# Performance work log

Measured on AMD Instinct MI355X. Metric: run time of the kernel, lower is better.

## Reference

```python
import jax, jax.numpy as jnp
import numpy as np

H = 187          # BATTLEFIELD_HEXES
MS = 20          # MAX_STACKS
MOB = 10         # MAX_OBSTACLES
D = 128          # d_model
NH = 4           # n_heads
NL = 4           # n_layers
CE = 16          # creature_embed_dim
NAT = 5          # NUM_ACTION_TYPES
NCT = 256        # NUM_CREATURE_TYPES
HEXC = 29        # HEX_CONTINUOUS_DIM
B = 1024


def _ln(x, g, b):
    m = x.mean(-1, keepdims=True)
    v = jnp.mean((x - m) ** 2, -1, keepdims=True)
    return (x - m) / jnp.sqrt(v + 1e-5) * g + b


def _mlp(x, w1, b1, w2, b2):
    return jax.nn.relu(x @ w1.T + b1) @ w2.T + b2


def _forward(p, n_stacks):
    scalars = p['scalars']
    s = p['stacks']
    pos = s[:, :, 18].astype(jnp.int32)                       # POSITION
    alive = s[:, :, 23]                                       # ALIVE
    idx_mask = jnp.arange(MS)[None, :] < n_stacks             # (B, MS)
    valid = (pos >= 0) & (pos < H) & (alive >= 0.5) & idx_mask
    max_hp = jnp.maximum(s[:, :, 4], 1.0)
    is_active = (s[:, :, 0] == scalars[:, 2:3]).astype(jnp.float32)
    is_ally = (s[:, :, 20] == scalars[:, 3:4]).astype(jnp.float32)
    zeros = jnp.zeros_like(alive)
    feat = jnp.stack([
        jnp.ones_like(alive), s[:, :, 2] / 1000.0, s[:, :, 3] / max_hp,
        s[:, :, 8] / 100.0, s[:, :, 9] / 100.0, s[:, :, 10] / 100.0, s[:, :, 11] / 100.0,
        s[:, :, 12] / 100.0, s[:, :, 13] / 100.0, s[:, :, 14] / 100.0, s[:, :, 15] / 100.0,
        s[:, :, 16] / 20.0, s[:, :, 17] / 20.0, s[:, :, 20], is_ally, alive,
        s[:, :, 24], s[:, :, 25], s[:, :, 26], s[:, :, 27], s[:, :, 28], s[:, :, 29],
        s[:, :, 30], s[:, :, 31] / 30.0, s[:, :, 33] / 5.0, s[:, :, 34] / 10.0,
        is_active, zeros, zeros], axis=-1)                    # (B, MS, 29)
    bidx = jnp.arange(B)[:, None]
    safe_pos = jnp.where(valid, pos, H)                       # dummy slot H for invalid
    hex_cont = jnp.zeros((B, H + 1, HEXC)).at[bidx, safe_pos].set(
        jnp.where(valid[..., None], feat, 0.0))[:, :H]
    cid = jnp.minimum(s[:, :, 1].astype(jnp.int32), NCT - 1)
    cids = jnp.zeros((B, H + 1), jnp.int32).at[bidx, safe_pos].set(
        jnp.where(valid, cid, 0))[:, :H]
    hex_cont = hex_cont.at[:, :, 27].set(p['reachable_hexes'])
    opos = p['obstacles'][:, :, 2].astype(jnp.int32)
    ovalid = (p['obstacles'][:, :, 0] > 0) & (opos >= 0) & (opos < H)
    obs_ch = jnp.zeros((B, H + 1)).at[bidx, jnp.where(ovalid, opos, H)].max(
        ovalid.astype(jnp.float32))[:, :H]
    hex_cont = hex_cont.at[:, :, 28].set(obs_ch)
    hex_feat = jnp.concatenate([hex_cont, p['creature_emb'][cids]], -1)   # (B,H,45)

    hex_tok = _ln(hex_feat @ p['hex_proj_w'].T + p['hex_proj_b'],
                  p['hex_ln_g'], p['hex_ln_b'])
    hex_tok = hex_tok + p['hex_pos_emb'][None] + p['tok_type_emb'][0]

    sc = scalars
    atk = jnp.stack([sc[:, 8], sc[:, 11] / 300.0, sc[:, 10] / 10.0, sc[:, 12] / 10.0,
                     jnp.zeros(B)], -1)
    dfn = jnp.stack([sc[:, 14], sc[:, 17] / 300.0, sc[:, 16] / 10.0, sc[:, 18] / 10.0,
                     jnp.ones(B)], -1)
    atk_t = _ln(atk @ p['hero_proj_w'].T + p['hero_proj_b'], p['hero_ln_g'], p['hero_ln_b']) + p['tok_type_emb'][1]
    def_t = _ln(dfn @ p['hero_proj_w'].T + p['hero_proj_b'], p['hero_ln_g'], p['hero_ln_b']) + p['tok_type_emb'][2]
    tokens = jnp.concatenate([hex_tok, atk_t[:, None], def_t[:, None]], 1)  # (B,189,D)

    gfeat = jnp.stack([sc[:, 1] / 50.0, sc[:, 4] / 10.0, sc[:, 5] / 10.0, sc[:, 6], sc[:, 3]], -1)
    tokens = tokens + (gfeat @ p['global_w'].T + p['global_b'])[:, None]

    S = tokens.shape[1]
    hd = D // NH
    for l in range(NL):  # pre-LN transformer encoder (eval mode, no dropout)
        x = _ln(tokens, p['tf_ln1_g'][l], p['tf_ln1_b'][l])
        qkv = x @ p['tf_qkv_w'][l].T + p['tf_qkv_b'][l]
        q, k, v = jnp.split(qkv, 3, -1)
        rs = lambda t: t.reshape(B, S, NH, hd).transpose(0, 2, 1, 3)
        q, k, v = rs(q), rs(k), rs(v)
        att = jax.nn.softmax(jnp.einsum('bhqd,bhkd->bhqk', q, k) / jnp.sqrt(float(hd)), -1)
        o = jnp.einsum('bhqk,bhkd->bhqd', att, v).transpose(0, 2, 1, 3).reshape(B, S, D)
        tokens = tokens + o @ p['tf_o_w'][l].T + p['tf_o_b'][l]
        y = _ln(tokens, p['tf_ln2_g'][l], p['tf_ln2_b'][l])
        tokens = tokens + jax.nn.relu(y @ p['tf_ff1_w'][l].T + p['tf_ff1_b'][l]) @ p['tf_ff2_w'][l].T + p['tf_ff2_b'][l]
    tokens = _ln(tokens, p['post_ln_g'], p['post_ln_b'])

    hex_out = tokens[:, :H]
    pooled = tokens.mean(1)
    action_type_logits = _mlp(pooled, p['at_w1'], p['at_b1'], p['at_w2'], p['at_b2'])
    hex_logits = _mlp(hex_out, p['hex_w1'], p['hex_b1'], p['hex_w2'], p['hex_b2']).squeeze(-1)
    tgt_tok = jnp.take_along_axis(hex_out, jnp.clip(pos, 0, H - 1)[..., None], axis=1)  # (B,MS,D)
    tgt = _mlp(tgt_tok, p['tg_w1'], p['tg_b1'], p['tg_w2'], p['tg_b2']).squeeze(-1)
    target_logits = jnp.where(valid, tgt, -1e9)
    value = _mlp(pooled, p['val_w1'], p['val_b1'], p['val_w2'], p['val_b2']).squeeze(-1)
    return (action_type_logits, hex_logits, target_logits, value)


def setup_inputs() -> dict:
    key = jax.random.key(0)
    ks = iter(jax.random.split(key, 64))
    nk = lambda: next(ks)
    _p = lambda shape: 0.02 * jax.random.normal(nk(), shape, dtype=jnp.float32)

    scalars = jax.random.uniform(nk(), (B, 19)) * 10.0
    scalars = scalars.at[:, 2].set(jax.random.randint(nk(), (B,), 0, MS).astype(jnp.float32))
    scalars = scalars.at[:, 3].set(jax.random.randint(nk(), (B,), 0, 2).astype(jnp.float32))

    stacks = jax.random.uniform(nk(), (B, MS, 35)) * 50.0
    perm = jax.vmap(lambda k: jax.random.permutation(k, H)[:MS])(jax.random.split(nk(), B))
    stacks = stacks.at[:, :, 18].set(perm.astype(jnp.float32))          # unique positions
    stacks = stacks.at[:, :, 23].set((jax.random.uniform(nk(), (B, MS)) > 0.2).astype(jnp.float32))
    stacks = stacks.at[:, :, 1].set(jax.random.randint(nk(), (B, MS), 0, NCT).astype(jnp.float32))
    stacks = stacks.at[:, :, 0].set(jnp.broadcast_to(jnp.arange(MS, dtype=jnp.float32), (B, MS)))
    stacks = stacks.at[:, :, 20].set(jax.random.randint(nk(), (B, MS), 0, 2).astype(jnp.float32))

    obstacles = jnp.stack([
        jax.random.randint(nk(), (B, MOB), 0, 3).astype(jnp.float32),
        jnp.zeros((B, MOB)),
        jax.random.randint(nk(), (B, MOB), 0, H).astype(jnp.float32)], -1)
    reachable_hexes = (jax.random.uniform(nk(), (B, H)) > 0.5).astype(jnp.float32)
    n_stacks = jax.random.randint(nk(), (B, 1), 1, MS + 1)

    inp = dict(scalars=scalars, stacks=stacks, obstacles=obstacles,
               reachable_hexes=reachable_hexes, n_stacks=n_stacks)
    inp['creature_emb'] = _p((NCT, CE)).at[0].set(0.0)   # padding_idx=0
    inp['hex_pos_emb'] = _p((H, D))
    inp['tok_type_emb'] = _p((3, D))
    inp['hex_proj_w'] = _p((D, HEXC + CE)); inp['hex_proj_b'] = _p((D,))
    inp['hex_ln_g'] = jnp.ones(D); inp['hex_ln_b'] = jnp.zeros(D)
    inp['hero_proj_w'] = _p((D, 5)); inp['hero_proj_b'] = _p((D,))
    inp['hero_ln_g'] = jnp.ones(D); inp['hero_ln_b'] = jnp.zeros(D)
    inp['global_w'] = _p((D, 5)); inp['global_b'] = _p((D,))
    inp['tf_ln1_g'] = jnp.ones((NL, D)); inp['tf_ln1_b'] = jnp.zeros((NL, D))
    inp['tf_qkv_w'] = _p((NL, 3 * D, D)); inp['tf_qkv_b'] = _p((NL, 3 * D))
    inp['tf_o_w'] = _p((NL, D, D)); inp['tf_o_b'] = _p((NL, D))
    inp['tf_ln2_g'] = jnp.ones((NL, D)); inp['tf_ln2_b'] = jnp.zeros((NL, D))
    inp['tf_ff1_w'] = _p((NL, 4 * D, D)); inp['tf_ff1_b'] = _p((NL, 4 * D))
    inp['tf_ff2_w'] = _p((NL, D, 4 * D)); inp['tf_ff2_b'] = _p((NL, D))
    inp['post_ln_g'] = jnp.ones(D); inp['post_ln_b'] = jnp.zeros(D)
    inp['at_w1'] = _p((D, D)); inp['at_b1'] = _p((D,)); inp['at_w2'] = _p((NAT, D)); inp['at_b2'] = _p((NAT,))
    inp['hex_w1'] = _p((D // 2, D)); inp['hex_b1'] = _p((D // 2,)); inp['hex_w2'] = _p((1, D // 2)); inp['hex_b2'] = _p((1,))
    inp['tg_w1'] = _p((D // 2, D)); inp['tg_b1'] = _p((D // 2,)); inp['tg_w2'] = _p((1, D // 2)); inp['tg_b2'] = _p((1,))
    inp['val_w1'] = _p((D, D)); inp['val_b1'] = _p((D,)); inp['val_w2'] = _p((1, D)); inp['val_b2'] = _p((1,))
    return inp


def reference(scalars, stacks, obstacles, reachable_hexes, n_stacks, creature_emb, hex_pos_emb, tok_type_emb, hex_proj_w, hex_proj_b, hex_ln_g, hex_ln_b, hero_proj_w, hero_proj_b, hero_ln_g, hero_ln_b, global_w, global_b, tf_ln1_g, tf_ln1_b, tf_qkv_w, tf_qkv_b, tf_o_w, tf_o_b, tf_ln2_g, tf_ln2_b, tf_ff1_w, tf_ff1_b, tf_ff2_w, tf_ff2_b, post_ln_g, post_ln_b, at_w1, at_b1, at_w2, at_b2, hex_w1, hex_b1, hex_w2, hex_b2, tg_w1, tg_b1, tg_w2, tg_b2, val_w1, val_b1, val_w2, val_b2):
    fl = dict(locals())
    ns = fl.pop('n_stacks')
    return _forward(fl, ns)
```

## Files before the change

kernel.cpp:

```cpp
#include <hip/hip_runtime.h>
#include <hip/hip_bf16.h>

#define DEV static __device__ __forceinline__

typedef __attribute__((ext_vector_type(8))) short bf16x8;
typedef __attribute__((ext_vector_type(4))) float f32x4;
#define MFMA16 __builtin_amdgcn_mfma_f32_16x16x32_bf16

DEV unsigned short f2bf_rn(float x) {
  unsigned u = __float_as_uint(x);
  u = u + 0x7fffu + ((u >> 16) & 1u);
  return (unsigned short)(u >> 16);
}
DEV unsigned pack2(float a, float b) {
  return (unsigned)f2bf_rn(a) | ((unsigned)f2bf_rn(b) << 16);
}
DEV float lo2f(unsigned w) { return __uint_as_float(w << 16); }
DEV float hi2f(unsigned w) { return __uint_as_float(w & 0xffff0000u); }

constexpr int H_ = 187, MS_ = 20, MOB_ = 10, D_ = 128, NH_ = 4, NL_ = 4,
              CE_ = 16, NAT_ = 5, NCT_ = 256, HEXC_ = 29, B_ = 1024;
constexpr int S_ = H_ + 2;
constexpr int ST = 68;
constexpr int PST = 36;
// ... 16 lines not shown
constexpr int WS_Q = 0;
constexpr int WS_O = WS_Q + 4 * 384 * 128;
constexpr int WS_F1 = WS_O + 4 * 128 * 128;
constexpr int WS_F2 = WS_F1 + 4 * 512 * 128;
constexpr int WS_TOT = WS_F2 + 4 * 128 * 512;

struct Params {
  const float *scalars, *stacks, *obstacles, *reach;
  const int  *n_stacks;
  const float *cemb, *pos_emb, *tte;
  const float *hexW, *hexB, *hexG, *hexBe;
  const float *heroW, *heroB, *heroG, *heroBe;
  const float *gW, *gB;
  const float *ln1g, *ln1b, *qkvW, *qkvB, *oW, *oB;
  const float *ln2g, *ln2b, *f1W, *f1B, *f2W, *f2B;
  const float *plng, *plnb;
  const float *atW1, *atB1, *atW2, *atB2;
  const float *hxW1, *hxB1, *hxW2, *hxB2;
  const float *tgW1, *tgB1, *tgW2, *tgB2;
  const float *vlW1, *vlB1, *vlW2, *vlB2;
  const unsigned short *wsb;
  float *out;
};

DEV bf16x8 ldAx(const unsigned* buf, int stride, int mbase, int cbase, int lane) {
  return *(const bf16x8*)(buf + (mbase + (lane & 15)) * stride + cbase +
                          ((lane >> 4) << 2));
}
DEV bf16x8 ldBw(const float* q) {
  bf16x8 r;
#pragma unroll
  for (int j = 0; j < 8; ++j) r[j] = (short)f2bf_rn(q[j]);
  return r;
}
template <bool WSB>
DEV bf16x8 ldB(const unsigned short* wb, const float* wf, int off) {
  if constexpr (WSB) return *(const bf16x8*)(wb + off);
  else return ldBw(wf + off);
}

__global__ __launch_bounds__(256) void convw_kernel(const float *qkv,
                                                    const float *o,
                                                    const float *f1,
                                                    const float *f2,
                                                    unsigned short *ws) {
  int i = blockIdx.x * 256 + threadIdx.x;
  if (i < WS_O) ws[i] = f2bf_rn(qkv[i - WS_Q]);
  else if (i < WS_F1) ws[i] = f2bf_rn(o[i - WS_O]);
  else if (i < WS_F2) ws[i] = f2bf_rn(f1[i - WS_F1]);
  else if (i < WS_TOT) ws[i] = f2bf_rn(f2[i - WS_F2]);
}

template <bool WSB>
__global__ __launch_bounds__(384, 1) void battle_kernel(Params p) {
  __shared__ __align__(16) unsigned tokp[192 * ST];
  __shared__ __align__(16) unsigned xln[192 * ST];
  __shared__ __align__(16) unsigned area[192 * ST];
  __shared__ int svalid[MS_], sposc[MS_];

  const int b = blockIdx.x;
  const int tid = threadIdx.x;
  const int lane = tid & 63;
  const int wave = tid >> 6;
  const bool hasrow = tid < S_;
  const float *sc = p.scalars + b * 19;

  float *areaF = (float *)area;
  unsigned short *tok16 = (unsigned short *)tokp;
  unsigned short *xln16 = (unsigned short *)xln;
  unsigned short *P16 = (unsigned short *)area;
  unsigned short *vt16 = (unsigned short *)(area + VT_OFF);

  float *hexcont = (float *)area;
  int   *cids    = (int *)area + 5440;
  float *obsch   = (float *)area + 5632;

  if (tid < D_) {
    float g0 = sc[1] * 0.02f, g1 = sc[4] * 0.1f, g2 = sc[5] * 0.1f;
    float g3 = sc[6], g4 = sc[3];
    const float *w = p.gW + tid * 5;
    areaF[GV_OFF + tid] = p.gB[tid] + g0 * w[0] + g1 * w[1] + g2 * w[2] +
                          g3 * w[3] + g4 * w[4];
  }
  for (int i = tid; i < H_ * HEXC_; i += 384) hexcont[i] = 0.f;
  for (int i = tid; i < H_; i += 384) { cids[i] = 0; obsch[i] = 0.f; }
  if (tid >= 189 && tid < 192) {
    for (int c = 0; c < 64; ++c) tokp[tid * ST + c] = 0u;
  }
  __syncthreads();

  if (tid < MS_) {
    const float *st = p.stacks + (b * MS_ + tid) * 35;
    int pos = (int)st[18];
    float alive = st[23];
    int ns = p.n_stacks[b];
    bool valid = (pos >= 0) && (pos < H_) && (alive >= 0.5f) && (tid < ns);
    svalid[tid] = valid ? 1 : 0;
    sposc[tid] = min(max(pos, 0), H_ - 1);
    if (valid) {
      float maxhp = fmaxf(st[4], 1.0f);
      float *hc = hexcont + pos * HEXC_;
      hc[0] = 1.0f;
      hc[1] = st[2] * 1e-3f;
      hc[2] = st[3] / maxhp;
      hc[3] = st[8] * 0.01f;  hc[4] = st[9] * 0.01f;
      hc[5] = st[10] * 0.01f; hc[6] = st[11] * 0.01f;
      hc[7] = st[12] * 0.01f; hc[8] = st[13] * 0.01f;
      hc[9] = st[14] * 0.01f; hc[10] = st[15] * 0.01f;
      hc[11] = st[16] * 0.05f; hc[12] = st[17] * 0.05f;
      float s20 = st[20];
      hc[13] = s20;
      hc[14] = (s20 == sc[3]) ? 1.f : 0.f;
      hc[15] = alive;
      hc[16] = st[24]; hc[17] = st[25]; hc[18] = st[26];
      hc[19] = st[27]; hc[20] = st[28]; hc[21] = st[29];
      hc[22] = st[30];
      hc[23] = st[31] * (1.f / 30.f);
      hc[24] = st[33] * 0.2f;
      hc[25] = st[34] * 0.1f;
      hc[26] = (st[0] == sc[2]) ? 1.f : 0.f;
      hc[27] = 0.f; hc[28] = 0.f;
      cids[pos] = min((int)st[1], NCT_ - 1);
    }
  }
  if (tid >= 64 && tid < 64 + MOB_) {
    const float *ob = p.obstacles + (b * MOB_ + (tid - 64)) * 3;
    int opos = (int)ob[2];
    if (ob[0] > 0.f && opos >= 0 && opos < H_) obsch[opos] = 1.0f;
  }
  __syncthreads();

  if (tid < H_) {
    const int r = tid;
    float f[HEXC_ + CE_];
#pragma unroll
    for (int c = 0; c < HEXC_; ++c) f[c] = hexcont[r * HEXC_ + c];
    f[27] = p.reach[b * H_ + r];
    f[28] = obsch[r];
// ... 27 lines not shown
      float t0 = lo2f(w) - m, t1 = hi2f(w) - m;
      var = fmaf(t0, t0, var); var = fmaf(t1, t1, var);
    }
    float rs = rsqrtf(var * (1.f / 128.f) + 1e-5f);
#pragma unroll 2
    for (int d2 = 0; d2 < 64; ++d2) {
      unsigned w = tokp[r * ST + d2];
      int d = 2 * d2;
      float v0 = (lo2f(w) - m) * rs * p.hexG[d] + p.hexBe[d] +
                 p.pos_emb[r * D_ + d] + p.tte[d] + areaF[GV_OFF + d];
      float v1 = (hi2f(w) - m) * rs * p.hexG[d + 1] + p.hexBe[d + 1] +
                 p.pos_emb[r * D_ + d + 1] + p.tte[d + 1] + areaF[GV_OFF + d + 1];
      tokp[r * ST + d2] = pack2(v0, v1);
    }
  } else if (tid < S_) {
    const int which = tid - H_;
    float f0, f1, f2, f3, f4;
    if (which == 0) {
      f0 = sc[8];  f1 = sc[11] * (1.f / 300.f);
      f2 = sc[10] * 0.1f; f3 = sc[12] * 0.1f; f4 = 0.f;
    } else {
      f0 = sc[14]; f1 = sc[17] * (1.f / 300.f);
      f2 = sc[16] * 0.1f; f3 = sc[18] * 0.1f; f4 = 1.f;
    }
    const int r = tid;
    float sum = 0.f;
    for (int d2 = 0; d2 < 64; ++d2) {
      const float *w0 = p.heroW + (2 * d2) * 5;
      const float *w1 = w0 + 5;
      float va = p.heroB[2 * d2] + f0 * w0[0] + f1 * w0[1] + f2 * w0[2] + f3 * w0[3] + f4 * w0[4];
      float vb = p.heroB[2 * d2 + 1] + f0 * w1[0] + f1 * w1[1] + f2 * w1[2] + f3 * w1[3] + f4 * w1[4];
      tokp[r * ST + d2] = pack2(va, vb);
      sum += va + vb;
    }
    float m = sum * (1.f / 128.f);
    float var = 0.f;
    for (int d2 = 0; d2 < 64; ++d2) {
      unsigned w = tokp[r * ST + d2];
      float t0 = lo2f(w) - m, t1 = hi2f(w) - m;
      var = fmaf(t0, t0, var); var = fmaf(t1, t1, var);
    }
    float rs = rsqrtf(var * (1.f / 128.f) + 1e-5f);
    for (int d2 = 0; d2 < 64; ++d2) {
      unsigned w = tokp[r * ST + d2];
      int d = 2 * d2;
      float v0 = (lo2f(w) - m) * rs * p.heroG[d] + p.heroBe[d] +
                 p.tte[(1 + which) * D_ + d] + areaF[GV_OFF + d];
      float v1 = (hi2f(w) - m) * rs * p.heroG[d + 1] + p.heroBe[d + 1] +
                 p.tte[(1 + which) * D_ + d + 1] + areaF[GV_OFF + d + 1];
      tokp[r * ST + d2] = pack2(v0, v1);
    }
  }

  for (int l = 0; l < NL_; ++l) {
    const float *ln1g = p.ln1g + l * D_, *ln1b = p.ln1b + l * D_;
    const float *qkvW = p.qkvW + l * 3 * D_ * D_, *qkvB = p.qkvB + l * 3 * D_;
    const float *oW = p.oW + l * D_ * D_, *oB = p.oB + l * D_;
    const float *ln2g = p.ln2g + l * D_, *ln2b = p.ln2b + l * D_;
    const float *f1W = p.f1W + l * 4 * D_ * D_, *f1B = p.f1B + l * 4 * D_;
    const float *f2W = p.f2W + l * 4 * D_ * D_, *f2B = p.f2B + l * D_;
    const unsigned short *qkvWb = p.wsb + WS_Q + l * 384 * 128;
    const unsigned short *oWb = p.wsb + WS_O + l * 128 * 128;
    const unsigned short *f1Wb = p.wsb + WS_F1 + l * 512 * 128;
    const unsigned short *f2Wb = p.wsb + WS_F2 + l * 128 * 512;

    __syncthreads();

    if (hasrow) {
      float s0 = 0.f, s1 = 0.f;
#pragma unroll 8
      for (int d2 = 0; d2 < 64; ++d2) {
        unsigned w = tokp[tid * ST + d2];
        s0 += lo2f(w); s1 += hi2f(w);
      }
      float m = (s0 + s1) * (1.f / 128.f);
      float v0 = 0.f, v1 = 0.f;
#pragma unroll 8
      for (int d2 = 0; d2 < 64; ++d2) {
        unsigned w = tokp[tid * ST + d2];
        float t0 = lo2f(w) - m, t1 = hi2f(w) - m;
        v0 = fmaf(t0, t0, v0); v1 = fmaf(t1, t1, v1);
      }
      float rs = rsqrtf((v0 + v1) * (1.f / 128.f) + 1e-5f);
#pragma unroll 2
      for (int d2 = 0; d2 < 64; ++d2) {
        unsigned w = tokp[tid * ST + d2];
        int d = 2 * d2;
        xln[tid * ST + d2] = pack2((lo2f(w) - m) * rs * ln1g[d] + ln1b[d],
                                   (hi2f(w) - m) * rs * ln1g[d + 1] + ln1b[d + 1]);
      }
    } else if (tid < 192) {
      for (int d2 = 0; d2 < 64; ++d2) xln[tid * ST + d2] = 0u;
    }
    __syncthreads();

    f32x4 oacc[4][2][2];

#pragma unroll
    for (int h = 0; h < NH_; ++h) {
#pragma unroll
      for (int mi = 0; mi < 2; ++mi)
#pragma unroll
        for (int nd = 0; nd < 2; ++nd) oacc[h][mi][nd] = {0.f, 0.f, 0.f, 0.f};

      {
        int job = wave;
        int nrow0, c16 = 0, isV = 0, ntd = 0;
        if (job < 2)      { nrow0 = h * 32 + job * 16;            c16 = job * 16; }
        else if (job < 4) { nrow0 = 128 + h * 32 + (job - 2) * 16; c16 = 32 + (job - 2) * 16; }
        else              { nrow0 = 256 + h * 32 + (job - 4) * 16; isV = 1; ntd = job - 4; }
        int roff = (nrow0 + (lane & 15)) * 128;
        int koff = (lane >> 4) << 3;
        bf16x8 b0 = ldB<WSB>(qkvWb, qkvW, roff + koff);
        bf16x8 b1 = ldB<WSB>(qkvWb, qkvW, roff + 32 + koff);
        bf16x8 b2 = ldB<WSB>(qkvWb, qkvW, roff + 64 + koff);
        bf16x8 b3 = ldB<WSB>(qkvWb, qkvW, roff + 96 + koff);
        float bv = qkvB[nrow0 + (lane & 15)];
        int col16 = c16 + (lane & 15);
#pragma unroll 1
        for (int mt = 0; mt < 12; ++mt) {
          f32x4 acc = {bv, bv, bv, bv};
          acc = MFMA16(ldAx(xln, ST, mt * 16, 0, lane), b0, acc, 0, 0, 0);
          acc = MFMA16(ldAx(xln, ST, mt * 16, 16, lane), b1, acc, 0, 0, 0);
          acc = MFMA16(ldAx(xln, ST, mt * 16, 32, lane), b2, acc, 0, 0, 0);
          acc = MFMA16(ldAx(xln, ST, mt * 16, 48, lane), b3, acc, 0, 0, 0);
          int rb = mt * 16 + ((lane >> 4) << 2);
          if (!isV) {
#pragma unroll
            for (int g = 0; g < 4; ++g)
              P16[(rb + g) * (PST * 2) + col16] = f2bf_rn(acc[g]);
          } else {
#pragma unroll
            for (int g = 0; g < 4; ++g)
              vt16[(ntd * 16 + (lane & 15)) * (VTS * 2) + rb + g] = f2bf_rn(acc[g]);
          }
        }
      }
      __syncthreads();

      bf16x8 qf0 = ldAx(area, PST, (2 * wave) * 16, 0, lane);
      bf16x8 qf1 = ldAx(area, PST, (2 * wave + 1) * 16, 0, lane);
      bf16x8 kf[12];
#pragma unroll
      for (int nt = 0; nt < 12; ++nt)
        kf[nt] = ldAx(area, PST, nt * 16, 16, lane);
      float mrun = -1e30f, lrun = 0.f;
      const int srow = 32 * wave + (lane & 31);
      const int shalf = lane >> 5;
      __syncthreads();

#pragma unroll
      for (int t = 0; t < 3; ++t) {
#pragma unroll
        for (int mi = 0; mi < 2; ++mi) {
          int rb = (2 * wave + mi) * 16 + ((lane >> 4) << 2);
#pragma unroll
          for (int ntl = 0; ntl < 4; ++ntl) {
            f32x4 s = {0.f, 0.f, 0.f, 0.f};
            s = MFMA16(mi ? qf1 : qf0, kf[t * 4 + ntl], s, 0, 0, 0);
            int col16 = ntl * 16 + (lane & 15);
#pragma unroll
            for (int g = 0; g < 4; ++g)
              P16[(rb + g) * (PST * 2) + col16] = f2bf_rn(s[g]);
          }
        }
        {
          float tm = -1e30f;
          int cb = shalf * 16;
#pragma unroll
          for (int c2i = 0; c2i < 16; ++c2i) {
            int c2 = cb + c2i;
            unsigned w = area[srow * PST + c2];
            float v0 = lo2f(w) * SCALE, v1 = hi2f(w) * SCALE;
            if (t == 2 && c2 == 30) v1 = -1e30f;
            if (t == 2 && c2 == 31) { v0 = -1e30f; v1 = -1e30f; }
            tm = fmaxf(tm, fmaxf(v0, v1));
          }
          tm = fmaxf(tm, __shfl_xor(tm, 32));
          float mnew = fmaxf(mrun, tm);
          float corrv = __expf(mrun - mnew);
          float ts = 0.f;
#pragma unroll
          for (int c2i = 0; c2i < 16; ++c2i) {
            int c2 = cb + c2i;
            unsigned w = area[srow * PST + c2];
            float e0 = __expf(lo2f(w) * SCALE - mnew);
            float e1 = __expf(hi2f(w) * SCALE - mnew);
            if (t == 2 && c2 == 30) e1 = 0.f;
            if (t == 2 && c2 == 31) { e0 = 0.f; e1 = 0.f; }
            ts += e0 + e1;
            area[srow * PST + c2] = pack2(e0, e1);
          }
          ts += __shfl_xor(ts, 32);
          lrun = lrun * corrv + ts;
          mrun = mnew;
          if (shalf == 0) {
            areaF[CORR_OFF + srow] = corrv;
            if (t == 2) areaF[LSUM_OFF + srow] = lrun;
          }
        }
#pragma unroll
        for (int mi = 0; mi < 2; ++mi) {
          int rb = (2 * wave + mi) * 16 + ((lane >> 4) << 2);
          float c0 = areaF[CORR_OFF + rb], c1 = areaF[CORR_OFF + rb + 1];
          float c2v = areaF[CORR_OFF + rb + 2], c3 = areaF[CORR_OFF + rb + 3];
#pragma unroll
          for (int nd = 0; nd < 2; ++nd) {
            f32x4 a = oacc[h][mi][nd];
            a[0] *= c0; a[1] *= c1; a[2] *= c2v; a[3] *= c3;
#pragma unroll
            for (int kt = 0; kt < 2; ++kt) {
              bf16x8 af = ldAx(area, PST, (2 * wave + mi) * 16, kt * 16, lane);
              bf16x8 bv = *(const bf16x8*)(area + VT_OFF +
                            (nd * 16 + (lane & 15)) * VTS + t * 32 + kt * 16 +
                            ((lane >> 4) << 2));
              a = MFMA16(af, bv, a, 0, 0, 0);
            }
            oacc[h][mi][nd] = a;
          }
          if (t == 2) {
            float i0 = 1.f / areaF[LSUM_OFF + rb];
            float i1 = 1.f / areaF[LSUM_OFF + rb + 1];
            float i2 = 1.f / areaF[LSUM_OFF + rb + 2];
            float i3 = 1.f / areaF[LSUM_OFF + rb + 3];
#pragma unroll
            for (int nd = 0; nd < 2; ++nd) {
              f32x4 a = oacc[h][mi][nd];
              a[0] *= i0; a[1] *= i1; a[2] *= i2; a[3] *= i3;
              oacc[h][mi][nd] = a;
            }
          }
        }
      }
      __syncthreads();
    }

#pragma unroll
    for (int h = 0; h < NH_; ++h)
#pragma unroll
      for (int mi = 0; mi < 2; ++mi) {
        int rb = (2 * wave + mi) * 16 + ((lane >> 4) << 2);
#pragma unroll
        for (int nd = 0; nd < 2; ++nd) {
          int col16 = h * 32 + nd * 16 + (lane & 15);
          f32x4 a = oacc[h][mi][nd];
#pragma unroll
          for (int g = 0; g < 4; ++g)
            xln16[(rb + g) * (ST * 2) + col16] = f2bf_rn(a[g]);
        }
      }
    __syncthreads();

#pragma unroll 1
    for (int job = wave; job < 16; job += 6) {
      int nt = job >> 1, mh = job & 1;
      int roff = (nt * 16 + (lane & 15)) * 128;
      int koff = (lane >> 4) << 3;
      bf16x8 b0 = ldB<WSB>(oWb, oW, roff + koff);
      bf16x8 b1 = ldB<WSB>(oWb, oW, roff + 32 + koff);
      bf16x8 b2 = ldB<WSB>(oWb, oW, roff + 64 + koff);
      bf16x8 b3 = ldB<WSB>(oWb, oW, roff + 96 + koff);
      float bv = oB[nt * 16 + (lane & 15)];
      int col16 = nt * 16 + (lane & 15);
#pragma unroll 1
      for (int mt = mh * 6; mt < mh * 6 + 6; ++mt) {
        f32x4 acc = {bv, bv, bv, bv};
        acc = MFMA16(ldAx(xln, ST, mt * 16, 0, lane), b0, acc, 0, 0, 0);
        acc = MFMA16(ldAx(xln, ST, mt * 16, 16, lane), b1, acc, 0, 0, 0);
        acc = MFMA16(ldAx(xln, ST, mt * 16, 32, lane), b2, acc, 0, 0, 0);
        acc = MFMA16(ldAx(xln, ST, mt * 16, 48, lane), b3, acc, 0, 0, 0);
        int rb = mt * 16 + ((lane >> 4) << 2);
#pragma unroll
        for (int g = 0; g < 4; ++g) {
          int a16 = (rb + g) * (ST * 2) + col16;
          float old = __uint_as_float((unsigned)tok16[a16] << 16);
          tok16[a16] = f2bf_rn(old + acc[g]);
        }
      }
    }
    __syncthreads();

    if (hasrow) {
      float s0 = 0.f, s1 = 0.f;
#pragma unroll 8
      for (int d2 = 0; d2 < 64; ++d2) {
        unsigned w = tokp[tid * ST + d2];
        s0 += lo2f(w); s1 += hi2f(w);
      }
      float m = (s0 + s1) * (1.f / 128.f);
      float v0 = 0.f, v1 = 0.f;
#pragma unroll 8
      for (int d2 = 0; d2 < 64; ++d2) {
        unsigned w = tokp[tid * ST + d2];
        float t0 = lo2f(w) - m, t1 = hi2f(w) - m;
        v0 = fmaf(t0, t0, v0); v1 = fmaf(t1, t1, v1);
      }
      float rs = rsqrtf((v0 + v1) * (1.f / 128.f) + 1e-5f);
#pragma unroll 2
      for (int d2 = 0; d2 < 64; ++d2) {
        unsigned w = tokp[tid * ST + d2];
        int d = 2 * d2;
        xln[tid * ST + d2] = pack2((lo2f(w) - m) * rs * ln2g[d] + ln2b[d],
                                   (hi2f(w) - m) * rs * ln2g[d + 1] + ln2b[d + 1]);
      }
    } else if (tid < 192) {
      for (int d2 = 0; d2 < 64; ++d2) xln[tid * ST + d2] = 0u;
    }
    __syncthreads();

    f32x4 acc2[2][12];
#pragma unroll
    for (int o = 0; o < 2; ++o) {
      int nt = wave + 6 * o;
      float bv = (nt < 8) ? f2B[nt * 16 + (lane & 15)] : 0.f;
#pragma unroll
      for (int mt = 0; mt < 12; ++mt) acc2[o][mt] = {bv, bv, bv, bv};
    }
    for (int chunk = 0; chunk < 4; ++chunk) {
#pragma unroll 1
      for (int job = wave; job < 16; job += 6) {
        int nt = job >> 1, mh = job & 1;
        int roff = (chunk * 128 + nt * 16 + (lane & 15)) * 128;
        int koff = (lane >> 4) << 3;
        bf16x8 b0 = ldB<WSB>(f1Wb, f1W, roff + koff);
        bf16x8 b1 = ldB<WSB>(f1Wb, f1W, roff + 32 + koff);
        bf16x8 b2 = ldB<WSB>(f1Wb, f1W, roff + 64 + koff);
        bf16x8 b3 = ldB<WSB>(f1Wb, f1W, roff + 96 + koff);
        float bv = f1B[chunk * 128 + nt * 16 + (lane & 15)];
        int col16 = nt * 16 + (lane & 15);
#pragma unroll 1
        for (int mt = mh * 6; mt < mh * 6 + 6; ++mt) {
          f32x4 acc = {bv, bv, bv, bv};
          acc = MFMA16(ldAx(xln, ST, mt * 16, 0, lane), b0, acc, 0, 0, 0);
          acc = MFMA16(ldAx(xln, ST, mt * 16, 16, lane), b1, acc, 0, 0, 0);
          acc = MFMA16(ldAx(xln, ST, mt * 16, 32, lane), b2, acc, 0, 0, 0);
          acc = MFMA16(ldAx(xln, ST, mt * 16, 48, lane), b3, acc, 0, 0, 0);
          int rb = mt * 16 + ((lane >> 4) << 2);
#pragma unroll
          for (int g = 0; g < 4; ++g)
            P16[(rb + g) * (ST * 2) + col16] = f2bf_rn(fmaxf(acc[g], 0.f));
        }
      }
      __syncthreads();
#pragma unroll
      for (int o = 0; o < 2; ++o) {
        int nt = wave + 6 * o;
        if (nt < 8) {
          int roff = (nt * 16 + (lane & 15)) * 512 + chunk * 128;
          int koff = (lane >> 4) << 3;
          bf16x8 b0 = ldB<WSB>(f2Wb, f2W, roff + koff);
          bf16x8 b1 = ldB<WSB>(f2Wb, f2W, roff + 32 + koff);
          bf16x8 b2 = ldB<WSB>(f2Wb, f2W, roff + 64 + koff);
          bf16x8 b3 = ldB<WSB>(f2Wb, f2W, roff + 96 + koff);
#pragma unroll
          for (int mt = 0; mt < 12; ++mt) {
            f32x4 a = acc2[o][mt];
            a = MFMA16(ldAx(area, ST, mt * 16, 0, lane), b0, a, 0, 0, 0);
            a = MFMA16(ldAx(area, ST, mt * 16, 16, lane), b1, a, 0, 0, 0);
            a = MFMA16(ldAx(area, ST, mt * 16, 32, lane), b2, a, 0, 0, 0);
            a = MFMA16(ldAx(area, ST, mt * 16, 48, lane), b3, a, 0, 0, 0);
            acc2[o][mt] = a;
          }
        }
      }
      __syncthreads();
    }
#pragma unroll
    for (int o = 0; o < 2; ++o) {
      int nt = wave + 6 * o;
      if (nt < 8) {
        int col16 = nt * 16 + (lane & 15);
#pragma unroll
        for (int mt = 0; mt < 12; ++mt) {
          int rb = mt * 16 + ((lane >> 4) << 2);
          f32x4 a = acc2[o][mt];
#pragma unroll
          for (int g = 0; g < 4; ++g) {
            int a16 = (rb + g) * (ST * 2) + col16;
            float old = __uint_as_float((unsigned)tok16[a16] << 16);
            tok16[a16] = f2bf_rn(old + a[g]);
          }
        }
      }
    }
  }
  __syncthreads();

  if (hasrow) {
    float s0 = 0.f, s1 = 0.f;
#pragma unroll 8
    for (int d2 = 0; d2 < 64; ++d2) {
      unsigned w = tokp[tid * ST + d2];
      s0 += lo2f(w); s1 += hi2f(w);
    }
    float m = (s0 + s1) * (1.f / 128.f);
    float v0 = 0.f, v1 = 0.f;
#pragma unroll 8
    for (int d2 = 0; d2 < 64; ++d2) {
      unsigned w = tokp[tid * ST + d2];
      float t0 = lo2f(w) - m, t1 = hi2f(w) - m;
      v0 = fmaf(t0, t0, v0); v1 = fmaf(t1, t1, v1);
    }
    float rs = rsqrtf((v0 + v1) * (1.f / 128.f) + 1e-5f);
#pragma unroll 2
    for (int d2 = 0; d2 < 64; ++d2) {
      unsigned w = tokp[tid * ST + d2];
      int d = 2 * d2;
      tokp[tid * ST + d2] = pack2((lo2f(w) - m) * rs * p.plng[d] + p.plnb[d],
                                  (hi2f(w) - m) * rs * p.plng[d + 1] + p.plnb[d + 1]);
    }
  }
  __syncthreads();

  if (tid < D_) {
    const int d2 = tid >> 1;
    const bool hi = tid & 1;
    float s0 = 0.f, s1 = 0.f;
    int r = 0;
    for (; r + 2 <= S_; r += 2) {
      unsigned w0 = tokp[r * ST + d2], w1 = tokp[(r + 1) * ST + d2];
      s0 += hi ? hi2f(w0) : lo2f(w0);
      s1 += hi ? hi2f(w1) : lo2f(w1);
    }
    unsigned wl = tokp[(S_ - 1) * ST + d2];
    s0 += hi ? hi2f(wl) : lo2f(wl);
    areaF[PO_OFF + tid] = (s0 + s1) * (1.f / (float)S_);
  }
  __syncthreads();
  if (tid < D_) {
    const float *wa = p.atW1 + tid * D_;
    const float *wv = p.vlW1 + tid * D_;
    float a0 = p.atB1[tid], a1 = 0.f, vv0 = p.vlB1[tid], vv1 = 0.f;
#pragma unroll 4
    for (int k = 0; k < D_; k += 2) {
      float pk0 = areaF[PO_OFF + k], pk1 = areaF[PO_OFF + k + 1];
      a0 = fmaf(pk0, wa[k], a0);   a1 = fmaf(pk1, wa[k + 1], a1);
      vv0 = fmaf(pk0, wv[k], vv0); vv1 = fmaf(pk1, wv[k + 1], vv1);
    }
    areaF[H1_OFF + tid] = fmaxf(a0 + a1, 0.f);
    areaF[H2_OFF + tid] = fmaxf(vv0 + vv1, 0.f);
  }
  __syncthreads();

  if (tid < H_) {
    float hh[64];
#pragma unroll
    for (int j = 0; j < 64; ++j) hh[j] = p.hxB1[j];
    for (int kb = 0; kb < 8; ++kb) {
      float xr[16];
#pragma unroll
      for (int i2 = 0; i2 < 8; ++i2) {
        unsigned w = tokp[tid * ST + kb * 8 + i2];
        xr[2 * i2] = lo2f(w); xr[2 * i2 + 1] = hi2f(w);
      }
      const float *w = p.hxW1 + kb * 16;
#pragma unroll
      for (int j = 0; j < 64; ++j) {
#pragma unroll
        for (int i = 0; i < 16; ++i)
          hh[j] = fmaf(xr[i], w[j * D_ + i], hh[j]);
      }
    }
// ... 47 lines not shown
          for (int i = 0; i < 16; ++i)
            hh[j] = fmaf(xr[i], w[j * D_ + i], hh[j]);
        }
      }
      o = p.tgB2[0];
#pragma unroll
      for (int j = 0; j < 64; ++j) o = fmaf(fmaxf(hh[j], 0.f), p.tgW2[j], o);
    } else {
      o = -1e9f;
    }
    p.out[OFF_TGT + b * MS_ + si] = o;
  }
}

extern "C" void kernel_launch(void* const* d_in, const int* in_sizes, int n_in,
                              void* d_out, int out_size, void* d_ws, size_t ws_size,
                              hipStream_t stream) {
  (void)in_sizes; (void)n_in; (void)out_size;
  Params p;
  p.scalars = (const float *)d_in[0];
  p.stacks = (const float *)d_in[1];
  p.obstacles = (const float *)d_in[2];
  p.reach = (const float *)d_in[3];
  p.n_stacks = (const int *)d_in[4];
  p.cemb = (const float *)d_in[5];
  p.pos_emb = (const float *)d_in[6];
  p.tte = (const float *)d_in[7];
  p.hexW = (const float *)d_in[8];  p.hexB = (const float *)d_in[9];
  p.hexG = (const float *)d_in[10]; p.hexBe = (const float *)d_in[11];
  p.heroW = (const float *)d_in[12]; p.heroB = (const float *)d_in[13];
  p.heroG = (const float *)d_in[14]; p.heroBe = (const float *)d_in[15];
  p.gW = (const float *)d_in[16]; p.gB = (const float *)d_in[17];
  p.ln1g = (const float *)d_in[18]; p.ln1b = (const float *)d_in[19];
  p.qkvW = (const float *)d_in[20]; p.qkvB = (const float *)d_in[21];
  p.oW = (const float *)d_in[22]; p.oB = (const float *)d_in[23];
  p.ln2g = (const float *)d_in[24]; p.ln2b = (const float *)d_in[25];
  p.f1W = (const float *)d_in[26]; p.f1B = (const float *)d_in[27];
  p.f2W = (const float *)d_in[28]; p.f2B = (const float *)d_in[29];
  p.plng = (const float *)d_in[30]; p.plnb = (const float *)d_in[31];
  p.atW1 = (const float *)d_in[32]; p.atB1 = (const float *)d_in[33];
  p.atW2 = (const float *)d_in[34]; p.atB2 = (const float *)d_in[35];
  p.hxW1 = (const float *)d_in[36]; p.hxB1 = (const float *)d_in[37];
  p.hxW2 = (const float *)d_in[38]; p.hxB2 = (const float *)d_in[39];
  p.tgW1 = (const float *)d_in[40]; p.tgB1 = (const float *)d_in[41];
  p.tgW2 = (const float *)d_in[42]; p.tgB2 = (const float *)d_in[43];
  p.vlW1 = (const float *)d_in[44]; p.vlB1 = (const float *)d_in[45];
  p.vlW2 = (const float *)d_in[46]; p.vlB2 = (const float *)d_in[47];
  p.out = (float *)d_out;
  bool usews = ws_size >= (size_t)WS_TOT * 2;
  if (usews) {
    p.wsb = (const unsigned short *)d_ws;
    convw_kernel<<<dim3((WS_TOT + 255) / 256), dim3(256), 0, stream>>>(
        p.qkvW, p.oW, p.f1W, p.f2W, (unsigned short *)d_ws);
    battle_kernel<true><<<dim3(B_), dim3(384), 0, stream>>>(p);
  } else {
    p.wsb = nullptr;
    battle_kernel<false><<<dim3(B_), dim3(384), 0, stream>>>(p);
  }
}
```

Before: 2.115 ms.

## Double block to 768 threads and repartition LN, attention and FFN work across 12 waves

Raises the block size from 384 to 768 threads, so 12 waves share each batch element instead of 6. LayerNorm now uses 4 threads per row with shuffle reductions rather than one thread per row. Attention gives each wave one 16-row tile, the QKV projection splits M tiles in half across wave pairs, and FF2 tiles are redistributed over 12 waves. This targets the serial per-row LayerNorm and low wave-level parallelism inside the block, at the cost of fewer registers per thread and more threads per barrier.

```diff
diff --git a/kernel.cpp b/kernel.cpp
--- a/kernel.cpp
+++ b/kernel.cpp
@@ -92,7 +92,7 @@
 }
 
 template <bool WSB>
-__global__ __launch_bounds__(384, 1) void battle_kernel(Params p) {
+__global__ __launch_bounds__(768, 1) void battle_kernel(Params p) {
   __shared__ __align__(16) unsigned tokp[192 * ST];
   __shared__ __align__(16) unsigned xln[192 * ST];
   __shared__ __align__(16) unsigned area[192 * ST];
@@ -122,8 +122,8 @@
     areaF[GV_OFF + tid] = p.gB[tid] + g0 * w[0] + g1 * w[1] + g2 * w[2] +
                           g3 * w[3] + g4 * w[4];
   }
-  for (int i = tid; i < H_ * HEXC_; i += 384) hexcont[i] = 0.f;
-  for (int i = tid; i < H_; i += 384) { cids[i] = 0; obsch[i] = 0.f; }
+  for (int i = tid; i < H_ * HEXC_; i += 768) hexcont[i] = 0.f;
+  for (int i = tid; i < H_; i += 768) { cids[i] = 0; obsch[i] = 0.f; }
   if (tid >= 189 && tid < 192) {
     for (int c = 0; c < 64; ++c) tokp[tid * ST + c] = 0u;
   }
@@ -257,6 +257,9 @@
     }
   }
 
+  const int lrow = tid >> 2;
+  const int lsub = tid & 3;
+
   for (int l = 0; l < NL_; ++l) {
     const float *ln1g = p.ln1g + l * D_, *ln1b = p.ln1b + l * D_;
     const float *qkvW = p.qkvW + l * 3 * D_ * D_, *qkvB = p.qkvB + l * 3 * D_;
@@ -271,49 +274,50 @@
 
     __syncthreads();
 
-    if (hasrow) {
-      float s0 = 0.f, s1 = 0.f;
-#pragma unroll 8
-      for (int d2 = 0; d2 < 64; ++d2) {
-        unsigned w = tokp[tid * ST + d2];
-        s0 += lo2f(w); s1 += hi2f(w);
-      }
-      float m = (s0 + s1) * (1.f / 128.f);
-      float v0 = 0.f, v1 = 0.f;
-#pragma unroll 8
-      for (int d2 = 0; d2 < 64; ++d2) {
-        unsigned w = tokp[tid * ST + d2];
+    if (lrow < S_) {
+      float s = 0.f;
+#pragma unroll
+      for (int i = 0; i < 16; ++i) {
+        unsigned w = tokp[lrow * ST + lsub * 16 + i];
+        s += lo2f(w) + hi2f(w);
+      }
+      s += __shfl_xor(s, 1); s += __shfl_xor(s, 2);
+      float m = s * (1.f / 128.f);
+      float v = 0.f;
+#pragma unroll
+      for (int i = 0; i < 16; ++i) {
+        unsigned w = tokp[lrow * ST + lsub * 16 + i];
         float t0 = lo2f(w) - m, t1 = hi2f(w) - m;
-        v0 = fmaf(t0, t0, v0); v1 = fmaf(t1, t1, v1);
-      }
-      float rs = rsqrtf((v0 + v1) * (1.f / 128.f) + 1e-5f);
-#pragma unroll 2
-      for (int d2 = 0; d2 < 64; ++d2) {
-        unsigned w = tokp[tid * ST + d2];
-        int d = 2 * d2;
-        xln[tid * ST + d2] = pack2((lo2f(w) - m) * rs * ln1g[d] + ln1b[d],
-                                   (hi2f(w) - m) * rs * ln1g[d + 1] + ln1b[d + 1]);
-      }
-    } else if (tid < 192) {
-      for (int d2 = 0; d2 < 64; ++d2) xln[tid * ST + d2] = 0u;
+        v = fmaf(t0, t0, v); v = fmaf(t1, t1, v);
+      }
+      v += __shfl_xor(v, 1); v += __shfl_xor(v, 2);
+      float rs = rsqrtf(v * (1.f / 128.f) + 1e-5f);
+#pragma unroll
+      for (int i = 0; i < 16; ++i) {
+        int d2 = lsub * 16 + i, d = 2 * d2;
+        unsigned w = tokp[lrow * ST + d2];
+        xln[lrow * ST + d2] = pack2((lo2f(w) - m) * rs * ln1g[d] + ln1b[d],
+                                    (hi2f(w) - m) * rs * ln1g[d + 1] + ln1b[d + 1]);
+      }
+    } else {
+#pragma unroll
+      for (int i = 0; i < 16; ++i) xln[lrow * ST + lsub * 16 + i] = 0u;
     }
     __syncthreads();
 
-    f32x4 oacc[4][2][2];
+    f32x4 oacc[4][2];
 
 #pragma unroll
     for (int h = 0; h < NH_; ++h) {
 #pragma unroll
-      for (int mi = 0; mi < 2; ++mi)
-#pragma unroll
-        for (int nd = 0; nd < 2; ++nd) oacc[h][mi][nd] = {0.f, 0.f, 0.f, 0.f};
+      for (int nd = 0; nd < 2; ++nd) oacc[h][nd] = {0.f, 0.f, 0.f, 0.f};
 
       {
-        int job = wave;
+        int ntg = wave >> 1, mh = wave & 1;
         int nrow0, c16 = 0, isV = 0, ntd = 0;
-        if (job < 2)      { nrow0 = h * 32 + job * 16;            c16 = job * 16; }
-        else if (job < 4) { nrow0 = 128 + h * 32 + (job - 2) * 16; c16 = 32 + (job - 2) * 16; }
-        else              { nrow0 = 256 + h * 32 + (job - 4) * 16; isV = 1; ntd = job - 4; }
+        if (ntg < 2)      { nrow0 = h * 32 + ntg * 16;            c16 = ntg * 16; }
+        else if (ntg < 4) { nrow0 = 128 + h * 32 + (ntg - 2) * 16; c16 = 32 + (ntg - 2) * 16; }
+        else              { nrow0 = 256 + h * 32 + (ntg - 4) * 16; isV = 1; ntd = ntg - 4; }
         int roff = (nrow0 + (lane & 15)) * 128;
         int koff = (lane >> 4) << 3;
         bf16x8 b0 = ldB<WSB>(qkvWb, qkvW, roff + koff);
@@ -323,7 +327,7 @@
         float bv = qkvB[nrow0 + (lane & 15)];
         int col16 = c16 + (lane & 15);
 #pragma unroll 1
-        for (int mt = 0; mt < 12; ++mt) {
+        for (int mt = mh * 6; mt < mh * 6 + 6; ++mt) {
           f32x4 acc = {bv, bv, bv, bv};
           acc = MFMA16(ldAx(xln, ST, mt * 16, 0, lane), b0, acc, 0, 0, 0);
           acc = MFMA16(ldAx(xln, ST, mt * 16, 16, lane), b1, acc, 0, 0, 0);
@@ -343,26 +347,24 @@
       }
       __syncthreads();
 
-      bf16x8 qf0 = ldAx(area, PST, (2 * wave) * 16, 0, lane);
-      bf16x8 qf1 = ldAx(area, PST, (2 * wave + 1) * 16, 0, lane);
+      bf16x8 qf = ldAx(area, PST, wave * 16, 0, lane);
       bf16x8 kf[12];
 #pragma unroll
       for (int nt = 0; nt < 12; ++nt)
         kf[nt] = ldAx(area, PST, nt * 16, 16, lane);
       float mrun = -1e30f, lrun = 0.f;
-      const int srow = 32 * wave + (lane & 31);
-      const int shalf = lane >> 5;
+      const int srow = wave * 16 + (lane & 15);
+      const int ssub = lane >> 4;
       __syncthreads();
 
 #pragma unroll
       for (int t = 0; t < 3; ++t) {
-#pragma unroll
-        for (int mi = 0; mi < 2; ++mi) {
-          int rb = (2 * wave + mi) * 16 + ((lane >> 4) << 2);
+        {
+          int rb = wave * 16 + ((lane >> 4) << 2);
 #pragma unroll
           for (int ntl = 0; ntl < 4; ++ntl) {
             f32x4 s = {0.f, 0.f, 0.f, 0.f};
-            s = MFMA16(mi ? qf1 : qf0, kf[t * 4 + ntl], s, 0, 0, 0);
+            s = MFMA16(qf, kf[t * 4 + ntl], s, 0, 0, 0);
             int col16 = ntl * 16 + (lane & 15);
 #pragma unroll
             for (int g = 0; g < 4; ++g)
@@ -371,23 +373,24 @@
         }
         {
           float tm = -1e30f;
-          int cb = shalf * 16;
-#pragma unroll
-          for (int c2i = 0; c2i < 16; ++c2i) {
-            int c2 = cb + c2i;
+          int cb = ssub * 8;
+#pragma unroll
+          for (int i = 0; i < 8; ++i) {
+            int c2 = cb + i;
             unsigned w = area[srow * PST + c2];
             float v0 = lo2f(w) * SCALE, v1 = hi2f(w) * SCALE;
             if (t == 2 && c2 == 30) v1 = -1e30f;
             if (t == 2 && c2 == 31) { v0 = -1e30f; v1 = -1e30f; }
             tm = fmaxf(tm, fmaxf(v0, v1));
           }
+          tm = fmaxf(tm, __shfl_xor(tm, 16));
           tm = fmaxf(tm, __shfl_xor(tm, 32));
           float mnew = fmaxf(mrun, tm);
           float corrv = __expf(mrun - mnew);
           float ts = 0.f;
 #pragma unroll
-          for (int c2i = 0; c2i < 16; ++c2i) {
-            int c2 = cb + c2i;
+          for (int i = 0; i < 8; ++i) {
+            int c2 = cb + i;
             unsigned w = area[srow * PST + c2];
             float e0 = __expf(lo2f(w) * SCALE - mnew);
             float e1 = __expf(hi2f(w) * SCALE - mnew);
@@ -396,32 +399,32 @@
             ts += e0 + e1;
             area[srow * PST + c2] = pack2(e0, e1);
           }
+          ts += __shfl_xor(ts, 16);
           ts += __shfl_xor(ts, 32);
           lrun = lrun * corrv + ts;
           mrun = mnew;
-          if (shalf == 0) {
+          if (ssub == 0) {
             areaF[CORR_OFF + srow] = corrv;
             if (t == 2) areaF[LSUM_OFF + srow] = lrun;
           }
         }
-#pragma unroll
-        for (int mi = 0; mi < 2; ++mi) {
-          int rb = (2 * wave + mi) * 16 + ((lane >> 4) << 2);
+        {
+          int rb = wave * 16 + ((lane >> 4) << 2);
           float c0 = areaF[CORR_OFF + rb], c1 = areaF[CORR_OFF + rb + 1];
           float c2v = areaF[CORR_OFF + rb + 2], c3 = areaF[CORR_OFF + rb + 3];
 #pragma unroll
           for (int nd = 0; nd < 2; ++nd) {
-            f32x4 a = oacc[h][mi][nd];
+            f32x4 a = oacc[h][nd];
             a[0] *= c0; a[1] *= c1; a[2] *= c2v; a[3] *= c3;
 #pragma unroll
             for (int kt = 0; kt < 2; ++kt) {
-              bf16x8 af = ldAx(area, PST, (2 * wave + mi) * 16, kt * 16, lane);
+              bf16x8 af = ldAx(area, PST, wave * 16, kt * 16, lane);
               bf16x8 bv = *(const bf16x8*)(area + VT_OFF +
                             (nd * 16 + (lane & 15)) * VTS + t * 32 + kt * 16 +
                             ((lane >> 4) << 2));
               a = MFMA16(af, bv, a, 0, 0, 0);
             }
-            oacc[h][mi][nd] = a;
+            oacc[h][nd] = a;
           }
           if (t == 2) {
             float i0 = 1.f / areaF[LSUM_OFF + rb];
@@ -430,9 +433,9 @@
             float i3 = 1.f / areaF[LSUM_OFF + rb + 3];
 #pragma unroll
             for (int nd = 0; nd < 2; ++nd) {
-              f32x4 a = oacc[h][mi][nd];
+              f32x4 a = oacc[h][nd];
               a[0] *= i0; a[1] *= i1; a[2] *= i2; a[3] *= i3;
-              oacc[h][mi][nd] = a;
+              oacc[h][nd] = a;
             }
           }
         }
@@ -441,23 +444,21 @@
     }
 
 #pragma unroll
-    for (int h = 0; h < NH_; ++h)
-#pragma unroll
-      for (int mi = 0; mi < 2; ++mi) {
-        int rb = (2 * wave + mi) * 16 + ((lane >> 4) << 2);
-#pragma unroll
-        for (int nd = 0; nd < 2; ++nd) {
-          int col16 = h * 32 + nd * 16 + (lane & 15);
-          f32x4 a = oacc[h][mi][nd];
-#pragma unroll
-          for (int g = 0; g < 4; ++g)
-            xln16[(rb + g) * (ST * 2) + col16] = f2bf_rn(a[g]);
-        }
-      }
+    for (int h = 0; h < NH_; ++h) {
+      int rb = wave * 16 + ((lane >> 4) << 2);
+#pragma unroll
+      for (int nd = 0; nd < 2; ++nd) {
+        int col16 = h * 32 + nd * 16 + (lane & 15);
+        f32x4 a = oacc[h][nd];
+#pragma unroll
+        for (int g = 0; g < 4; ++g)
+          xln16[(rb + g) * (ST * 2) + col16] = f2bf_rn(a[g]);
+      }
+    }
     __syncthreads();
 
 #pragma unroll 1
-    for (int job = wave; job < 16; job += 6) {
+    for (int job = wave; job < 16; job += 12) {
       int nt = job >> 1, mh = job & 1;
       int roff = (nt * 16 + (lane & 15)) * 128;
       int koff = (lane >> 4) << 3;
@@ -485,45 +486,54 @@
     }
     __syncthreads();
 
-    if (hasrow) {
-      float s0 = 0.f, s1 = 0.f;
-#pragma unroll 8
-      for (int d2 = 0; d2 < 64; ++d2) {
-        unsigned w = tokp[tid * ST + d2];
-        s0 += lo2f(w); s1 += hi2f(w);
-      }
-      float m = (s0 + s1) * (1.f / 128.f);
-      float v0 = 0.f, v1 = 0.f;
-#pragma unroll 8
-      for (int d2 = 0; d2 < 64; ++d2) {
-        unsigned w = tokp[tid * ST + d2];
+    if (lrow < S_) {
+      float s = 0.f;
+#pragma unroll
+      for (int i = 0; i < 16; ++i) {
+        unsigned w = tokp[lrow * ST + lsub * 16 + i];
+        s += lo2f(w) + hi2f(w);
+      }
+      s += __shfl_xor(s, 1); s += __shfl_xor(s, 2);
+      float m = s * (1.f / 128.f);
+      float v = 0.f;
+#pragma unroll
+      for (int i = 0; i < 16; ++i) {
+        unsigned w = tokp[lrow * ST + lsub * 16 + i];
         float t0 = lo2f(w) - m, t1 = hi2f(w) - m;
-        v0 = fmaf(t0, t0, v0); v1 = fmaf(t1, t1, v1);
-      }
-      float rs = rsqrtf((v0 + v1) * (1.f / 128.f) + 1e-5f);
-#pragma unroll 2
-      for (int d2 = 0; d2 < 64; ++d2) {
-        unsigned w = tokp[tid * ST + d2];
-        int d = 2 * d2;
-        xln[tid * ST + d2] = pack2((lo2f(w) - m) * rs * ln2g[d] + ln2b[d],
-                                   (hi2f(w) - m) * rs * ln2g[d + 1] + ln2b[d + 1]);
-      }
-    } else if (tid < 192) {
-      for (int d2 = 0; d2 < 64; ++d2) xln[tid * ST + d2] = 0u;
+        v = fmaf(t0, t0, v); v = fmaf(t1, t1, v);
+      }
+      v += __shfl_xor(v, 1); v += __shfl_xor(v, 2);
+      float rs = rsqrtf(v * (1.f / 128.f) + 1e-5f);
+#pragma unroll
+      for (int i = 0; i < 16; ++i) {
+        int d2 = lsub * 16 + i, d = 2 * d2;
+        unsigned w = tokp[lrow * ST + d2];
+        xln[lrow * ST + d2] = pack2((lo2f(w) - m) * rs * ln2g[d] + ln2b[d],
+                                    (hi2f(w) - m) * rs * ln2g[d + 1] + ln2b[d + 1]);
+      }
+    } else {
+#pragma unroll
+      for (int i = 0; i < 16; ++i) xln[lrow * ST + lsub * 16 + i] = 0u;
     }
     __syncthreads();
 
-    f32x4 acc2[2][12];
-#pragma unroll
-    for (int o = 0; o < 2; ++o) {
-      int nt = wave + 6 * o;
-      float bv = (nt < 8) ? f2B[nt * 16 + (lane & 15)] : 0.f;
-#pragma unroll
-      for (int mt = 0; mt < 12; ++mt) acc2[o][mt] = {bv, bv, bv, bv};
+    const int ja = wave;
+    const bool hasb = wave < 4;
+    const int jb = wave + 12;
+    const int nta = ja >> 1, mha = ja & 1;
+    const int ntb = jb >> 1, mhb = jb & 1;
+    f32x4 acca[6], accb[6];
+    {
+      float bva = f2B[nta * 16 + (lane & 15)];
+#pragma unroll
+      for (int i = 0; i < 6; ++i) acca[i] = {bva, bva, bva, bva};
+      float bvb = hasb ? f2B[ntb * 16 + (lane & 15)] : 0.f;
+#pragma unroll
+      for (int i = 0; i < 6; ++i) accb[i] = {bvb, bvb, bvb, bvb};
     }
     for (int chunk = 0; chunk < 4; ++chunk) {
 #pragma unroll 1
-      for (int job = wave; job < 16; job += 6) {
+      for (int job = wave; job < 16; job += 12) {
         int nt = job >> 1, mh = job & 1;
         int roff = (chunk * 128 + nt * 16 + (lane & 15)) * 128;
         int koff = (lane >> 4) << 3;
@@ -547,72 +557,99 @@
         }
       }
       __syncthreads();
-#pragma unroll
-      for (int o = 0; o < 2; ++o) {
-        int nt = wave + 6 * o;
-        if (nt < 8) {
-          int roff = (nt * 16 + (lane & 15)) * 512 + chunk * 128;
-          int koff = (lane >> 4) << 3;
-          bf16x8 b0 = ldB<WSB>(f2Wb, f2W, roff + koff);
-          bf16x8 b1 = ldB<WSB>(f2Wb, f2W, roff + 32 + koff);
-          bf16x8 b2 = ldB<WSB>(f2Wb, f2W, roff + 64 + koff);
-          bf16x8 b3 = ldB<WSB>(f2Wb, f2W, roff + 96 + koff);
-#pragma unroll
-          for (int mt = 0; mt < 12; ++mt) {
-            f32x4 a = acc2[o][mt];
-            a = MFMA16(ldAx(area, ST, mt * 16, 0, lane), b0, a, 0, 0, 0);
-            a = MFMA16(ldAx(area, ST, mt * 16, 16, lane), b1, a, 0, 0, 0);
-            a = MFMA16(ldAx(area, ST, mt * 16, 32, lane), b2, a, 0, 0, 0);
-            a = MFMA16(ldAx(area, ST, mt * 16, 48, lane), b3, a, 0, 0, 0);
-            acc2[o][mt] = a;
-          }
+      {
+        int roff = (nta * 16 + (lane & 15)) * 512 + chunk * 128;
+        int koff = (lane >> 4) << 3;
+        bf16x8 b0 = ldB<WSB>(f2Wb, f2W, roff + koff);
+        bf16x8 b1 = ldB<WSB>(f2Wb, f2W, roff + 32 + koff);
+        bf16x8 b2 = ldB<WSB>(f2Wb, f2W, roff + 64 + koff);
+        bf16x8 b3 = ldB<WSB>(f2Wb, f2W, roff + 96 + koff);
+#pragma unroll
+        for (int i = 0; i < 6; ++i) {
+          int mt = mha * 6 + i;
+          f32x4 a = acca[i];
+          a = MFMA16(ldAx(area, ST, mt * 16, 0, lane), b0, a, 0, 0, 0);
+          a = MFMA16(ldAx(area, ST, mt * 16, 16, lane), b1, a, 0, 0, 0);
+          a = MFMA16(ldAx(area, ST, mt * 16, 32, lane), b2, a, 0, 0, 0);
+          a = MFMA16(ldAx(area, ST, mt * 16, 48, lane), b3, a, 0, 0, 0);
+          acca[i] = a;
+        }
+      }
+      if (hasb) {
+        int roff = (ntb * 16 + (lane & 15)) * 512 + chunk * 128;
+        int koff = (lane >> 4) << 3;
+        bf16x8 b0 = ldB<WSB>(f2Wb, f2W, roff + koff);
+        bf16x8 b1 = ldB<WSB>(f2Wb, f2W, roff + 32 + koff);
+        bf16x8 b2 = ldB<WSB>(f2Wb, f2W, roff + 64 + koff);
+        bf16x8 b3 = ldB<WSB>(f2Wb, f2W, roff + 96 + koff);
+#pragma unroll
+        for (int i = 0; i < 6; ++i) {
+          int mt = mhb * 6 + i;
+          f32x4 a = accb[i];
+          a = MFMA16(ldAx(area, ST, mt * 16, 0, lane), b0, a, 0, 0, 0);
+          a = MFMA16(ldAx(area, ST, mt * 16, 16, lane), b1, a, 0, 0, 0);
+          a = MFMA16(ldAx(area, ST, mt * 16, 32, lane), b2, a, 0, 0, 0);
+          a = MFMA16(ldAx(area, ST, mt * 16, 48, lane), b3, a, 0, 0, 0);
+          accb[i] = a;
         }
       }
       __syncthreads();
     }
-#pragma unroll
-    for (int o = 0; o < 2; ++o) {
-      int nt = wave + 6 * o;
-      if (nt < 8) {
-        int col16 = nt * 16 + (lane & 15);
-#pragma unroll
-        for (int mt = 0; mt < 12; ++mt) {
-          int rb = mt * 16 + ((lane >> 4) << 2);
-          f32x4 a = acc2[o][mt];
-#pragma unroll
-          for (int g = 0; g < 4; ++g) {
-            int a16 = (rb + g) * (ST * 2) + col16;
-            float old = __uint_as_float((unsigned)tok16[a16] << 16);
-            tok16[a16] = f2bf_rn(old + a[g]);
-          }
+    {
+      int col16 = nta * 16 + (lane & 15);
+#pragma unroll
+      for (int i = 0; i < 6; ++i) {
+        int rb = (mha * 6 + i) * 16 + ((lane >> 4) << 2);
+        f32x4 a = acca[i];
+#pragma unroll
+        for (int g = 0; g < 4; ++g) {
+          int a16 = (rb + g) * (ST * 2) + col16;
+          float old = __uint_as_float((unsigned)tok16[a16] << 16);
+          tok16[a16] = f2bf_rn(old + a[g]);
+        }
+      }
+    }
+    if (hasb) {
+      int col16 = ntb * 16 + (lane & 15);
+#pragma unroll
+      for (int i = 0; i < 6; ++i) {
+        int rb = (mhb * 6 + i) * 16 + ((lane >> 4) << 2);
+        f32x4 a = accb[i];
+#pragma unroll
+        for (int g = 0; g < 4; ++g) {
+          int a16 = (rb + g) * (ST * 2) + col16;
+          float old = __uint_as_float((unsigned)tok16[a16] << 16);
+          tok16[a16] = f2bf_rn(old + a[g]);
         }
       }
     }
   }
   __syncthreads();
 
-  if (hasrow) {
-    float s0 = 0.f, s1 = 0.f;
-#pragma unroll 8
-    for (int d2 = 0; d2 < 64; ++d2) {
-      unsigned w = tokp[tid * ST + d2];
-      s0 += lo2f(w); s1 += hi2f(w);
-    }
-    float m = (s0 + s1) * (1.f / 128.f);
-    float v0 = 0.f, v1 = 0.f;
-#pragma unroll 8
-    for (int d2 = 0; d2 < 64; ++d2) {
-      unsigned w = tokp[tid * ST + d2];
+  if (lrow < S_) {
+    float s = 0.f;
+#pragma unroll
+    for (int i = 0; i < 16; ++i) {
+      unsigned w = tokp[lrow * ST + lsub * 16 + i];
+      s += lo2f(w) + hi2f(w);
+    }
+    s += __shfl_xor(s, 1); s += __shfl_xor(s, 2);
+    float m = s * (1.f / 128.f);
+    float v = 0.f;
+#pragma unroll
+    for (int i = 0; i < 16; ++i) {
+      unsigned w = tokp[lrow * ST + lsub * 16 + i];
       float t0 = lo2f(w) - m, t1 = hi2f(w) - m;
-      v0 = fmaf(t0, t0, v0); v1 = fmaf(t1, t1, v1);
-    }
-    float rs = rsqrtf((v0 + v1) * (1.f / 128.f) + 1e-5f);
-#pragma unroll 2
-    for (int d2 = 0; d2 < 64; ++d2) {
-      unsigned w = tokp[tid * ST + d2];
-      int d = 2 * d2;
-      tokp[tid * ST + d2] = pack2((lo2f(w) - m) * rs * p.plng[d] + p.plnb[d],
-                                  (hi2f(w) - m) * rs * p.plng[d + 1] + p.plnb[d + 1]);
+      v = fmaf(t0, t0, v); v = fmaf(t1, t1, v);
+    }
+    v += __shfl_xor(v, 1); v += __shfl_xor(v, 2);
+    float rs = rsqrtf(v * (1.f / 128.f) + 1e-5f);
+#pragma unroll
+    for (int i = 0; i < 16; ++i) {
+      int d2 = lsub * 16 + i, d = 2 * d2;
+      unsigned w = tokp[lrow * ST + d2];
+      tokp[lrow * ST + d2] = pack2((lo2f(w) - m) * rs * p.plng[d] + p.plnb[d],
+                                   (hi2f(w) - m) * rs * p.plng[d + 1] + p.plnb[d + 1]);
     }
   }
   __syncthreads();
@@ -766,9 +803,9 @@
     p.wsb = (const unsigned short *)d_ws;
     convw_kernel<<<dim3((WS_TOT + 255) / 256), dim3(256), 0, stream>>>(
         p.qkvW, p.oW, p.f1W, p.f2W, (unsigned short *)d_ws);
-    battle_kernel<true><<<dim3(B_), dim3(384), 0, stream>>>(p);
+    battle_kernel<true><<<dim3(B_), dim3(768), 0, stream>>>(p);
   } else {
     p.wsb = nullptr;
-    battle_kernel<false><<<dim3(B_), dim3(384), 0, stream>>>(p);
+    battle_kernel<false><<<dim3(B_), dim3(768), 0, stream>>>(p);
   }
 }
```

After: 2.085 ms, median of 3. No clear change (-1.4%).
